# Performance work log

Measured on AMD Instinct MI355X. Metric: run time of the kernel, lower is better.

Reference implementation:

```python
import jax, jax.numpy as jnp
import numpy as np

B, N, D = 4, 8192, 128
H = 4 * D  # exp_factor * features
EPS = 1e-5


def layer_norm(x):
    # fresh nn.LayerNorm each call -> weight=1, bias=0 (no learned affine)
    mu = jnp.mean(x, axis=-1, keepdims=True)
    var = jnp.var(x, axis=-1, keepdims=True)
    return (x - mu) * jax.lax.rsqrt(var + EPS)


def setup_inputs() -> dict:
    key = jax.random.key(0)
    ks = jax.random.split(key, 8)
    x = jax.random.normal(ks[0], (B, N, D), dtype=jnp.float32)
    adj = jax.random.uniform(ks[1], (N, N), dtype=jnp.float32)
    attn_mask = jnp.ones((1,), dtype=jnp.int32)  # unused (torch masked_fill result discarded)
    pad_mask = jnp.ones((1,), dtype=jnp.int32)   # unused
    # FFN params (torch Linear default init scale ~ 1/sqrt(fan_in))
    w1 = jax.random.normal(ks[2], (D, H), dtype=jnp.float32) / np.sqrt(D)
    b1 = jnp.zeros((H,), dtype=jnp.float32)
    w2 = jax.random.normal(ks[3], (H, D), dtype=jnp.float32) / np.sqrt(H)
    b2 = jnp.zeros((D,), dtype=jnp.float32)
    return {"x": x, "adj": adj, "attn_mask": attn_mask, "pad_mask": pad_mask,
            "w1": w1, "b1": b1, "w2": w2, "b2": b2, "dim": 128}


def reference(x, adj, attn_mask, pad_mask, w1, b1, w2, b2, dim):
    # Sublayer 0: x + InrAwaSA(LN(x))
    h = layer_norm(x)                               # [B,N,D]
    # adj is provided -> scores = dense adj, shared across batch.
    # NOTE: masks are no-ops in the source (masked_fill not in-place).
    prob = jax.nn.softmax(adj, axis=-1)             # [N,N]
    attn_out = jnp.einsum('nm,bmd->bnd', prob, h)   # [B,N,D]
    x1 = x + attn_out
    # Sublayer 1: x1 + FFN(LN(x1))
    h1 = layer_norm(x1)
    ffn = jnp.maximum(h1 @ w1 + b1, 0.0) @ w2 + b2
    return x1 + ffn
```

## Files before the change

kernel.cpp:

```cpp
#include <hip/hip_runtime.h>
#include <hip/hip_bf16.h>

typedef __attribute__((ext_vector_type(8))) short bh8;
typedef __attribute__((ext_vector_type(4))) float fx4;
typedef __attribute__((ext_vector_type(8))) int i32x8;
typedef __attribute__((ext_vector_type(4))) int i32x4;

typedef const __attribute__((address_space(1))) unsigned int* gas_p;
typedef __attribute__((address_space(3))) unsigned int* las_p;

#define MFMA(a, b, c) __builtin_amdgcn_mfma_f32_16x16x32_bf16((a), (b), (c), 0, 0, 0)
#define MFMAS(a, b, c) __builtin_amdgcn_mfma_scale_f32_16x16x128_f8f6f4( \
    (a), (b), (c), 0, 0, 0, 0x7f7f7f7f, 0, 0x7f7f7f7f)

__device__ __forceinline__ unsigned short f2bf(float f) {
  unsigned u = __builtin_bit_cast(unsigned, f);
  u += 0x7fff + ((u >> 16) & 1);
  return (unsigned short)(u >> 16);
}

__device__ __forceinline__ float bflo2f(unsigned u) { return __builtin_bit_cast(float, u << 16); }

__device__ __forceinline__ void gld16(const void* g, void* l) {
  __builtin_amdgcn_global_load_lds((gas_p)g, (las_p)l, 16, 0, 0);
}

__global__ __launch_bounds__(256) void transpose_weights(const float* __restrict__ w1,
                                                         const float* __restrict__ w2,
                                                         unsigned short* __restrict__ w1t,
                                                         unsigned short* __restrict__ w2t) {
  const int tgl = blockIdx.x * 256 + threadIdx.x;
  { const int h = tgl >> 7, d = tgl & 127; w1t[tgl] = f2bf(w1[d * 512 + h]); }
  { const int d = tgl >> 9, h = tgl & 511; w2t[tgl] = f2bf(w2[h * 128 + d]); }
}

__global__ __launch_bounds__(256) void ln1_transpose(const float* __restrict__ x,
                                                     unsigned char* __restrict__ htf) {
  const int t = threadIdx.x, lane = t & 63, w = t >> 6;
  const int mt = blockIdx.x, b = blockIdx.y;
  __shared__ unsigned short tile[128 * 64];
  const float* xb = x + ((size_t)b * 8192 + (size_t)mt * 64) * 128;
  for (int it = 0; it < 16; ++it) {
    const int r = w * 16 + it;
    const float2 v = *(const float2*)(xb + r * 128 + lane * 2);
    float s = v.x + v.y, s2 = v.x * v.x + v.y * v.y;
    #pragma unroll
    for (int o = 1; o < 64; o <<= 1) { s += __shfl_xor(s, o); s2 += __shfl_xor(s2, o); }
    const float mean = s * 0.0078125f;
    const float var = s2 * 0.0078125f - mean * mean;
    const float rstd = rsqrtf(var + 1e-5f);
    const int mc = r >> 3, ml = r & 7;
    const int d0 = lane * 2, d1 = d0 + 1;
    tile[d0 * 64 + ((mc ^ (d0 & 7)) << 3) + ml] = f2bf((v.x - mean) * rstd);
    tile[d1 * 64 + ((mc ^ (d1 & 7)) << 3) + ml] = f2bf((v.y - mean) * rstd);
  }
  __syncthreads();
  #pragma unroll
  for (int i = 0; i < 4; ++i) {
    const int idx = i * 256 + t;
    const int d = idx >> 3, mc = idx & 7;
    const bh8 vv = *(const bh8*)(tile + d * 64 + ((mc ^ (d & 7)) << 3));
    int lo = 0, hi = 0;
    lo = __builtin_amdgcn_cvt_pk_fp8_f32(bflo2f((unsigned short)vv[0]),
                                         bflo2f((unsigned short)vv[1]), lo, false);
    lo = __builtin_amdgcn_cvt_pk_fp8_f32(bflo2f((unsigned short)vv[2]),
                                         bflo2f((unsigned short)vv[3]), lo, true);
    hi = __builtin_amdgcn_cvt_pk_fp8_f32(bflo2f((unsigned short)vv[4]),
                                         bflo2f((unsigned short)vv[5]), hi, false);
    hi = __builtin_amdgcn_cvt_pk_fp8_f32(bflo2f((unsigned short)vv[6]),
                                         bflo2f((unsigned short)vv[7]), hi, true);
    const int col = b * 128 + d;
    const int k0 = mt * 64 + mc * 8;
    const int frag = (k0 >> 7) * 32 + (col >> 4);
    const int off = ((col & 15) + 16 * ((k0 >> 5) & 3)) * 32 + (k0 & 31);
    *(uint2*)(htf + (size_t)frag * 2048 + off) = (uint2){(unsigned)lo, (unsigned)hi};
  }
}

__global__ __launch_bounds__(256, 2) void fused_attn(const float* __restrict__ adj,
                                                     const unsigned char* __restrict__ htf,
                                                     unsigned short* __restrict__ pbuf,
                                                     float* __restrict__ sden) {
  const int tid = threadIdx.x, lane = tid & 63, wn = tid >> 6;
  const int mt = blockIdx.x, z = blockIdx.y;
  const int kbase = z * 2048;

  __shared__ unsigned char Al[64 * 128];

  fx4 acc[4][8];
  #pragma unroll
  for (int i = 0; i < 4; ++i)
    #pragma unroll
    for (int j = 0; j < 8; ++j) acc[i][j] = (fx4){0.f, 0.f, 0.f, 0.f};

  i32x8 afr[4];

  const int ar = tid >> 2, aq = tid & 3;
  const float* aroot = adj + (size_t)(mt * 64 + ar) * 8192 + kbase;
  float sacc = 0.f;
  float4 a4[8];
  unsigned pk[8];

  auto issueAdj = [&](int tau) {
    #pragma unroll
    for (int j = 0; j < 8; ++j)
      a4[j] = *(const float4*)(aroot + tau * 128 + aq * 32 + j * 4);
  };
  auto expCvt = [&]() {
    #pragma unroll
    for (int j = 0; j < 8; ++j) {
      const float e0 = __expf(a4[j].x), e1 = __expf(a4[j].y);
      const float e2 = __expf(a4[j].z), e3 = __expf(a4[j].w);
      sacc += (e0 + e1) + (e2 + e3);
      int d = 0;
      d = __builtin_amdgcn_cvt_pk_fp8_f32(e0, e1, d, false);
      d = __builtin_amdgcn_cvt_pk_fp8_f32(e2, e3, d, true);
      pk[j] = (unsigned)d;
    }
  };
  auto writeA = [&]() {
    const i32x4 w0 = (i32x4){(int)pk[0], (int)pk[1], (int)pk[2], (int)pk[3]};
    const i32x4 w1 = (i32x4){(int)pk[4], (int)pk[5], (int)pk[6], (int)pk[7]};
    *(i32x4*)&Al[ar * 128 + (((aq * 2) ^ (ar & 7)) << 4)] = w0;
    *(i32x4*)&Al[ar * 128 + (((aq * 2 + 1) ^ (ar & 7)) << 4)] = w1;
  };
  auto ldAall = [&]() {
    #pragma unroll
    for (int mf = 0; mf < 4; ++mf) {
      const int rr = mf * 16 + (lane & 15);
      const int gb = (lane >> 4) * 2;
      const unsigned char* base = &Al[rr * 128];
      const i32x4 lo = *(const i32x4*)(base + ((gb ^ (rr & 7)) << 4));
      const i32x4 hi = *(const i32x4*)(base + (((gb + 1) ^ (rr & 7)) << 4));
      afr[mf] = (i32x8){lo.x, lo.y, lo.z, lo.w, hi.x, hi.y, hi.z, hi.w};
    }
  };

  issueAdj(0);
  expCvt();
  writeA();
  asm volatile("s_waitcnt lgkmcnt(0)" ::: "memory");
  __builtin_amdgcn_sched_barrier(0);
  __builtin_amdgcn_s_barrier();
  __builtin_amdgcn_sched_barrier(0);

  for (int tt = 0; tt < 16; ++tt) {
    ldAall();
    if (tt < 15) issueAdj(tt + 1);

    const int gkt = z * 16 + tt;
    const unsigned char* fb = htf + ((size_t)gkt * 32 + wn * 8) * 2048 + lane * 32;
    #pragma unroll
    for (int nf = 0; nf < 8; ++nf) {
      const unsigned char* fp = fb + nf * 2048;
      const i32x4 blo = *(const i32x4*)(fp);
      const i32x4 bhi = *(const i32x4*)(fp + 16);
      const i32x8 bfr = (i32x8){blo.x, blo.y, blo.z, blo.w, bhi.x, bhi.y, bhi.z, bhi.w};
      #pragma unroll
      for (int mf = 0; mf < 4; ++mf)
        acc[mf][nf] = MFMAS(afr[mf], bfr, acc[mf][nf]);
    }

    asm volatile("s_waitcnt lgkmcnt(0)" ::: "memory");
    __builtin_amdgcn_sched_barrier(0);
    __builtin_amdgcn_s_barrier();
    __builtin_amdgcn_sched_barrier(0);

    if (tt < 15) {
      expCvt();
      writeA();
      asm volatile("s_waitcnt lgkmcnt(0)" ::: "memory");
      __builtin_amdgcn_sched_barrier(0);
      __builtin_amdgcn_s_barrier();
      __builtin_amdgcn_sched_barrier(0);
    }
  }

  sacc += __shfl_xor(sacc, 1);
  sacc += __shfl_xor(sacc, 2);
  if (aq == 0) sden[(size_t)z * 8192 + mt * 64 + ar] = sacc;

  unsigned short* po = pbuf + (size_t)z * 8192 * 512;
  #pragma unroll
  for (int mf = 0; mf < 4; ++mf)
    #pragma unroll
    for (int nf = 0; nf < 8; ++nf) {
      const int col = wn * 128 + nf * 16 + (lane & 15);
      #pragma unroll
      for (int q = 0; q < 4; ++q) {
        const int row = mt * 64 + mf * 16 + (lane >> 4) * 4 + q;
        po[(size_t)row * 512 + col] = f2bf(acc[mf][nf][q]);
      }
    }
}

#define SWZ16(ks, r) (((((ks) & 7) ^ ((r) & 7)) | ((ks) & 8)))
__global__ __launch_bounds__(512) void ln_ffn_kernel(const float* __restrict__ x,
                                                     const unsigned short* __restrict__ pbuf,
                                                     const float* __restrict__ sden,
                                                     const unsigned short* __restrict__ w1t,
                                                     const unsigned short* __restrict__ w2t,
                                                     const float* __restrict__ b1,
                                                     const float* __restrict__ b2,
                                                     float* __restrict__ out) {
  const int t = threadIdx.x, lane = t & 63, w = t >> 6;
  const int wr = w >> 1, wc = w & 1;
  const int row0 = blockIdx.x * 128;
  __shared__ unsigned short As[128 * 128];
  __shared__ unsigned short W1c[128 * 128];
  __shared__ unsigned short W2c[128 * 128];
  __shared__ unsigned short Ts[128 * 128];

  auto stageW1 = [&](int hc) {
    #pragma unroll
    for (int i = 0; i < 4; ++i) {
      const int idx = i * 512 + t;
      const int row = idx >> 4, kc = idx & 15;
      const int kcs = (kc & 8) | ((kc & 7) ^ (row & 7));
      gld16(w1t + (size_t)(hc * 128 + row) * 128 + kcs * 8, W1c + (idx & ~63) * 8);
    }
  };
  auto stageW2 = [&](int hc) {
    #pragma unroll
    for (int i = 0; i < 4; ++i) {
      const int idx = i * 512 + t;
      const int row = idx >> 4, kc = idx & 15;
      const int kcs = (kc & 8) | ((kc & 7) ^ (row & 7));
      gld16(w2t + (size_t)row * 512 + hc * 128 + kcs * 8, W2c + (idx & ~63) * 8);
    }
  };

  stageW1(0); stageW2(0);

  const int r = t >> 2, q = t & 3, c0 = q * 32;
  const int rowg = row0 + r;
  const int bb = rowg >> 13, nn = rowg & 8191;
  float xv[32];
  {
    const float den = sden[nn] + sden[8192 + nn] + sden[16384 + nn] + sden[24576 + nn];
    const float rinv = 1.f / den;
    const float* xp = x + (size_t)rowg * 128 + c0;
    #pragma unroll
    for (int j = 0; j < 8; ++j) {
      const float4 v4 = *(const float4*)(xp + 4 * j);
      xv[4 * j] = v4.x; xv[4 * j + 1] = v4.y; xv[4 * j + 2] = v4.z; xv[4 * j + 3] = v4.w;
    }
    #pragma unroll
    for (int z = 0; z < 4; ++z) {
      const unsigned short* pp = pbuf + ((size_t)z * 8192 + nn) * 512 + bb * 128 + c0;
      #pragma unroll
      for (int j = 0; j < 4; ++j) {
        const bh8 pv = *(const bh8*)(pp + 8 * j);
        #pragma unroll
        for (int e = 0; e < 8; ++e) xv[8 * j + e] += bflo2f((unsigned short)pv[e]) * rinv;
      }
    }
  }
  float s = 0.f, s2 = 0.f;
  #pragma unroll
  for (int j = 0; j < 32; ++j) { s += xv[j]; s2 += xv[j] * xv[j]; }
  s += __shfl_xor(s, 1); s2 += __shfl_xor(s2, 1);
  s += __shfl_xor(s, 2); s2 += __shfl_xor(s2, 2);
  const float mean = s * 0.0078125f;
  const float var = s2 * 0.0078125f - mean * mean;
  const float rstd = rsqrtf(var + 1e-5f);
  #pragma unroll
  for (int j = 0; j < 4; ++j) {
    const int g = q * 4 + j;
    bh8 pk;
    #pragma unroll
    for (int e = 0; e < 8; ++e) pk[e] = (short)f2bf((xv[8 * j + e] - mean) * rstd);
    *(bh8*)(As + r * 128 + SWZ16(g, r) * 8) = pk;
  }
  __syncthreads();

  fx4 accO[2][4];
  #pragma unroll
  for (int i = 0; i < 2; ++i)
    #pragma unroll
    for (int j = 0; j < 4; ++j) accO[i][j] = (fx4){0.f, 0.f, 0.f, 0.f};

  for (int hc = 0; hc < 4; ++hc) {
    if (hc > 0) stageW2(hc);
    fx4 accT[2][4];
    #pragma unroll
    for (int i = 0; i < 2; ++i)
      #pragma unroll
      for (int j = 0; j < 4; ++j) accT[i][j] = (fx4){0.f, 0.f, 0.f, 0.f};
    #pragma unroll
    for (int kk = 0; kk < 4; ++kk) {
      const int ks = kk * 4 + (lane >> 4);
      bh8 af[2], bfr[4];
      #pragma unroll
      for (int f = 0; f < 2; ++f) {
        const int ra = wr * 32 + f * 16 + (lane & 15);
        af[f] = *(const bh8*)(As + ra * 128 + SWZ16(ks, ra) * 8);
      }
      #pragma unroll
      for (int f = 0; f < 4; ++f) {
        const int rb = wc * 64 + f * 16 + (lane & 15);
        bfr[f] = *(const bh8*)(W1c + rb * 128 + SWZ16(ks, rb) * 8);
      }
      #pragma unroll
      for (int fm = 0; fm < 2; ++fm)
        #pragma unroll
        for (int fn = 0; fn < 4; ++fn) accT[fm][fn] = MFMA(af[fm], bfr[fn], accT[fm][fn]);
    }
    #pragma unroll
    for (int fm = 0; fm < 2; ++fm)
      #pragma unroll
      for (int fn = 0; fn < 4; ++fn) {
        const int col = wc * 64 + fn * 16 + (lane & 15);
        const float bv = b1[hc * 128 + col];
        const int c = col >> 3;
        #pragma unroll
        for (int qq = 0; qq < 4; ++qq) {
          const int row = wr * 32 + fm * 16 + (lane >> 4) * 4 + qq;
          float vv = accT[fm][fn][qq] + bv;
          vv = fmaxf(vv, 0.f);
          Ts[row * 128 + SWZ16(c, row) * 8 + (col & 7)] = f2bf(vv);
        }
      }
    __syncthreads();
    if (hc < 3) {
      stageW1(hc + 1);
    } else {
      float* dst = (r < 64) ? (float*)As + r * 128 + c0 : (float*)W1c + (r - 64) * 128 + c0;
      #pragma unroll
      for (int j = 0; j < 8; ++j)
        *(float4*)(dst + 4 * j) =
            (float4){xv[4 * j], xv[4 * j + 1], xv[4 * j + 2], xv[4 * j + 3]};
    }
    #pragma unroll
    for (int kk = 0; kk < 4; ++kk) {
      const int ks = kk * 4 + (lane >> 4);
      bh8 af[2], bfr[4];
      #pragma unroll
      for (int f = 0; f < 2; ++f) {
        const int ra = wr * 32 + f * 16 + (lane & 15);
        af[f] = *(const bh8*)(Ts + ra * 128 + SWZ16(ks, ra) * 8);
      }
      #pragma unroll
      for (int f = 0; f < 4; ++f) {
        const int rb = wc * 64 + f * 16 + (lane & 15);
        bfr[f] = *(const bh8*)(W2c + rb * 128 + SWZ16(ks, rb) * 8);
      }
      #pragma unroll
      for (int fm = 0; fm < 2; ++fm)
        #pragma unroll
        for (int fn = 0; fn < 4; ++fn) accO[fm][fn] = MFMA(af[fm], bfr[fn], accO[fm][fn]);
    }
    __syncthreads();
  }

  const float* x1a = (const float*)As;
  const float* x1b = (const float*)W1c;
  float* op = out + (size_t)row0 * 128;
  #pragma unroll
  for (int fm = 0; fm < 2; ++fm)
    #pragma unroll
    for (int fn = 0; fn < 4; ++fn) {
      const int col = wc * 64 + fn * 16 + (lane & 15);
      const float bv = b2[col];
      #pragma unroll
      for (int qq = 0; qq < 4; ++qq) {
        const int row = wr * 32 + fm * 16 + (lane >> 4) * 4 + qq;
        const float x1v = (row < 64) ? x1a[row * 128 + col] : x1b[(row - 64) * 128 + col];
        op[row * 128 + col] = x1v + accO[fm][fn][qq] + bv;
      }
    }
}

extern "C" void kernel_launch(void* const* d_in, const int* in_sizes, int n_in,
                              void* d_out, int out_size, void* d_ws, size_t ws_size,
                              hipStream_t stream) {
  const float* x   = (const float*)d_in[0];
  const float* adj = (const float*)d_in[1];
  const float* w1  = (const float*)d_in[4];
  const float* b1  = (const float*)d_in[5];
  const float* w2  = (const float*)d_in[6];
  const float* b2  = (const float*)d_in[7];
  float* out = (float*)d_out;

  char* p = (char*)d_ws;
  unsigned short* w1t  = (unsigned short*)p; p += (size_t)512 * 128 * 2;
  unsigned short* w2t  = (unsigned short*)p; p += (size_t)128 * 512 * 2;
  unsigned char*  htf  = (unsigned char*)p;  p += (size_t)4 * 128 * 8192;
  unsigned short* pbuf = (unsigned short*)p; p += (size_t)4 * 8192 * 512 * 2;
  float*          sden = (float*)p;          p += (size_t)4 * 8192 * 4;

  transpose_weights<<<256, 256, 0, stream>>>(w1, w2, w1t, w2t);
  ln1_transpose<<<dim3(128, 4), 256, 0, stream>>>(x, htf);
  fused_attn<<<dim3(128, 4), 256, 0, stream>>>(adj, htf, pbuf, sden);
  ln_ffn_kernel<<<256, 512, 0, stream>>>(x, pbuf, sden, w1t, w2t, b1, b2, out);
}
```

Measured before the change: 162.9 us.

## Double-buffer adj tile in LDS and prefetch two tiles ahead

Splits the shared A tile into two LDS buffers and keeps two register sets of adj loads, so the next tile's exp/fp8 conversion and LDS write happen during the current tile's MFMA phase. This cuts one barrier per iteration and hides global-load latency by prefetching two k-steps ahead. It also changes the per-thread adj access pattern to interleaved float4 columns, which gives coalesced global reads, and writes LDS as 4-byte stores. The cost is more registers (two float4[8] sets) and twice the LDS, which could hurt occupancy at 2 blocks per CU.

```diff
diff --git a/kernel.cpp b/kernel.cpp
--- a/kernel.cpp
+++ b/kernel.cpp
@@ -85,7 +85,8 @@
   const int mt = blockIdx.x, z = blockIdx.y;
   const int kbase = z * 2048;
 
-  __shared__ unsigned char Al[64 * 128];
+  __shared__ unsigned char Al0[64 * 128];
+  __shared__ unsigned char Al1[64 * 128];
 
   fx4 acc[4][8];
   #pragma unroll
@@ -98,19 +99,19 @@
   const int ar = tid >> 2, aq = tid & 3;
   const float* aroot = adj + (size_t)(mt * 64 + ar) * 8192 + kbase;
   float sacc = 0.f;
-  float4 a4[8];
+  float4 a4a[8], a4b[8];
   unsigned pk[8];
 
-  auto issueAdj = [&](int tau) {
+  auto issueAdj = [&](float4 (&dst)[8], int tau) {
     #pragma unroll
     for (int j = 0; j < 8; ++j)
-      a4[j] = *(const float4*)(aroot + tau * 128 + aq * 32 + j * 4);
-  };
-  auto expCvt = [&]() {
+      dst[j] = *(const float4*)(aroot + tau * 128 + j * 16 + aq * 4);
+  };
+  auto expCvt = [&](const float4 (&src)[8]) {
     #pragma unroll
     for (int j = 0; j < 8; ++j) {
-      const float e0 = __expf(a4[j].x), e1 = __expf(a4[j].y);
-      const float e2 = __expf(a4[j].z), e3 = __expf(a4[j].w);
+      const float e0 = __expf(src[j].x), e1 = __expf(src[j].y);
+      const float e2 = __expf(src[j].z), e3 = __expf(src[j].w);
       sacc += (e0 + e1) + (e2 + e3);
       int d = 0;
       d = __builtin_amdgcn_cvt_pk_fp8_f32(e0, e1, d, false);
@@ -118,36 +119,23 @@
       pk[j] = (unsigned)d;
     }
   };
-  auto writeA = [&]() {
-    const i32x4 w0 = (i32x4){(int)pk[0], (int)pk[1], (int)pk[2], (int)pk[3]};
-    const i32x4 w1 = (i32x4){(int)pk[4], (int)pk[5], (int)pk[6], (int)pk[7]};
-    *(i32x4*)&Al[ar * 128 + (((aq * 2) ^ (ar & 7)) << 4)] = w0;
-    *(i32x4*)&Al[ar * 128 + (((aq * 2 + 1) ^ (ar & 7)) << 4)] = w1;
-  };
-  auto ldAall = [&]() {
+  auto writeA = [&](unsigned char* buf) {
+    #pragma unroll
+    for (int j = 0; j < 8; ++j)
+      *(unsigned*)&buf[ar * 128 + ((j ^ (ar & 7)) << 4) + aq * 4] = pk[j];
+  };
+  auto ldAall = [&](const unsigned char* buf) {
     #pragma unroll
     for (int mf = 0; mf < 4; ++mf) {
       const int rr = mf * 16 + (lane & 15);
       const int gb = (lane >> 4) * 2;
-      const unsigned char* base = &Al[rr * 128];
+      const unsigned char* base = &buf[rr * 128];
       const i32x4 lo = *(const i32x4*)(base + ((gb ^ (rr & 7)) << 4));
       const i32x4 hi = *(const i32x4*)(base + (((gb + 1) ^ (rr & 7)) << 4));
       afr[mf] = (i32x8){lo.x, lo.y, lo.z, lo.w, hi.x, hi.y, hi.z, hi.w};
     }
   };
-
-  issueAdj(0);
-  expCvt();
-  writeA();
-  asm volatile("s_waitcnt lgkmcnt(0)" ::: "memory");
-  __builtin_amdgcn_sched_barrier(0);
-  __builtin_amdgcn_s_barrier();
-  __builtin_amdgcn_sched_barrier(0);
-
-  for (int tt = 0; tt < 16; ++tt) {
-    ldAall();
-    if (tt < 15) issueAdj(tt + 1);
-
+  auto mfmaPhase = [&](int tt) {
     const int gkt = z * 16 + tt;
     const unsigned char* fb = htf + ((size_t)gkt * 32 + wn * 8) * 2048 + lane * 32;
     #pragma unroll
@@ -160,20 +148,35 @@
       for (int mf = 0; mf < 4; ++mf)
         acc[mf][nf] = MFMAS(afr[mf], bfr, acc[mf][nf]);
     }
-
+  };
+  auto body = [&](int tt, unsigned char* bufCur, unsigned char* bufNxt,
+                  float4 (&cur)[8], float4 (&nxt)[8]) {
+    ldAall(bufCur);
+    if (tt + 2 < 16) issueAdj(nxt, tt + 2);
+    if (tt + 1 < 16) {
+      expCvt(cur);
+      writeA(bufNxt);
+    }
+    mfmaPhase(tt);
     asm volatile("s_waitcnt lgkmcnt(0)" ::: "memory");
     __builtin_amdgcn_sched_barrier(0);
     __builtin_amdgcn_s_barrier();
     __builtin_amdgcn_sched_barrier(0);
-
-    if (tt < 15) {
-      expCvt();
-      writeA();
-      asm volatile("s_waitcnt lgkmcnt(0)" ::: "memory");
-      __builtin_amdgcn_sched_barrier(0);
-      __builtin_amdgcn_s_barrier();
-      __builtin_amdgcn_sched_barrier(0);
-    }
+  };
+
+  issueAdj(a4a, 0);
+  expCvt(a4a);
+  writeA(Al0);
+  issueAdj(a4a, 1);
+  asm volatile("s_waitcnt lgkmcnt(0)" ::: "memory");
+  __builtin_amdgcn_sched_barrier(0);
+  __builtin_amdgcn_s_barrier();
+  __builtin_amdgcn_sched_barrier(0);
+
+  for (int i = 0; i < 8; ++i) {
+    const int t0 = 2 * i;
+    body(t0, Al0, Al1, a4a, a4b);
+    body(t0 + 1, Al1, Al0, a4b, a4a);
   }
 
   sacc += __shfl_xor(sacc, 1);
```

Result: slower. 376.8 us (+131.4%).

## Stage adj tiles into double-buffered LDS via async global-to-LDS loads

Applied to the files above, without the earlier changes.

The adj tile loads move from register float4 loads to global_load_lds copies into a double-buffered fp32 LDS staging area with a swizzled layout, prefetched two tiles ahead. The fp8 A-tile buffer is also double-buffered, so the exp/convert step for the next tile runs in the same iteration as the MFMA phase for the current one, leaving one barrier per iteration instead of two. The goal is to hide adj load latency and cut synchronisation. In exchange it uses about 80KB of LDS per block, which could limit occupancy. Each wave only waits on its own vmcnt before reading staging rows that other waves filled, which risks a cross-wave race.

```diff
diff --git a/kernel.cpp b/kernel.cpp
--- a/kernel.cpp
+++ b/kernel.cpp
@@ -85,7 +85,8 @@
   const int mt = blockIdx.x, z = blockIdx.y;
   const int kbase = z * 2048;
 
-  __shared__ unsigned char Al[64 * 128];
+  __shared__ float Ar[2][64 * 128];
+  __shared__ unsigned char Al[2][64 * 128];
 
   fx4 acc[4][8];
   #pragma unroll
@@ -96,21 +97,28 @@
   i32x8 afr[4];
 
   const int ar = tid >> 2, aq = tid & 3;
-  const float* aroot = adj + (size_t)(mt * 64 + ar) * 8192 + kbase;
   float sacc = 0.f;
-  float4 a4[8];
   unsigned pk[8];
 
-  auto issueAdj = [&](int tau) {
-    #pragma unroll
-    for (int j = 0; j < 8; ++j)
-      a4[j] = *(const float4*)(aroot + tau * 128 + aq * 32 + j * 4);
-  };
-  auto expCvt = [&]() {
+  auto issueAr = [&](int buf, int tau) {
+    const int l = tid & 63, wid = tid >> 6;
+    #pragma unroll
+    for (int c = 0; c < 8; ++c) {
+      const int r = c * 8 + wid * 2 + (l >> 5);
+      const int p = l & 31;
+      const float* src = adj + (size_t)(mt * 64 + r) * 8192 + kbase + tau * 128
+                         + ((p ^ (r & 7)) << 2);
+      gld16(src, (char*)&Ar[buf][0] + c * 4096 + wid * 1024);
+    }
+  };
+  auto expCvt = [&](int buf) {
     #pragma unroll
     for (int j = 0; j < 8; ++j) {
-      const float e0 = __expf(a4[j].x), e1 = __expf(a4[j].y);
-      const float e2 = __expf(a4[j].z), e3 = __expf(a4[j].w);
+      const int g = j * 4 + aq;
+      const float4 v = *(const float4*)((const char*)&Ar[buf][0] + ar * 512 +
+                                        ((g ^ (ar & 7)) << 4));
+      const float e0 = __expf(v.x), e1 = __expf(v.y);
+      const float e2 = __expf(v.z), e3 = __expf(v.w);
       sacc += (e0 + e1) + (e2 + e3);
       int d = 0;
       d = __builtin_amdgcn_cvt_pk_fp8_f32(e0, e1, d, false);
@@ -118,36 +126,23 @@
       pk[j] = (unsigned)d;
     }
   };
-  auto writeA = [&]() {
-    const i32x4 w0 = (i32x4){(int)pk[0], (int)pk[1], (int)pk[2], (int)pk[3]};
-    const i32x4 w1 = (i32x4){(int)pk[4], (int)pk[5], (int)pk[6], (int)pk[7]};
-    *(i32x4*)&Al[ar * 128 + (((aq * 2) ^ (ar & 7)) << 4)] = w0;
-    *(i32x4*)&Al[ar * 128 + (((aq * 2 + 1) ^ (ar & 7)) << 4)] = w1;
-  };
-  auto ldAall = [&]() {
+  auto writeA = [&](int buf) {
+    #pragma unroll
+    for (int j = 0; j < 8; ++j)
+      *(unsigned*)&Al[buf][ar * 128 + ((j ^ (ar & 7)) << 4) + aq * 4] = pk[j];
+  };
+  auto ldAall = [&](int buf) {
     #pragma unroll
     for (int mf = 0; mf < 4; ++mf) {
       const int rr = mf * 16 + (lane & 15);
       const int gb = (lane >> 4) * 2;
-      const unsigned char* base = &Al[rr * 128];
+      const unsigned char* base = &Al[buf][rr * 128];
       const i32x4 lo = *(const i32x4*)(base + ((gb ^ (rr & 7)) << 4));
       const i32x4 hi = *(const i32x4*)(base + (((gb + 1) ^ (rr & 7)) << 4));
       afr[mf] = (i32x8){lo.x, lo.y, lo.z, lo.w, hi.x, hi.y, hi.z, hi.w};
     }
   };
-
-  issueAdj(0);
-  expCvt();
-  writeA();
-  asm volatile("s_waitcnt lgkmcnt(0)" ::: "memory");
-  __builtin_amdgcn_sched_barrier(0);
-  __builtin_amdgcn_s_barrier();
-  __builtin_amdgcn_sched_barrier(0);
-
-  for (int tt = 0; tt < 16; ++tt) {
-    ldAall();
-    if (tt < 15) issueAdj(tt + 1);
-
+  auto mfmaPhase = [&](int tt) {
     const int gkt = z * 16 + tt;
     const unsigned char* fb = htf + ((size_t)gkt * 32 + wn * 8) * 2048 + lane * 32;
     #pragma unroll
@@ -160,21 +155,44 @@
       for (int mf = 0; mf < 4; ++mf)
         acc[mf][nf] = MFMAS(afr[mf], bfr, acc[mf][nf]);
     }
-
+  };
+  auto body = [&](int tt, bool doIssue, bool doConv) {
+    const int cur = tt & 1;
+    if (doIssue) issueAr(cur, tt + 2);
+    ldAall(cur);
+    mfmaPhase(tt);
+    if (doConv) {
+      if (doIssue) { asm volatile("s_waitcnt vmcnt(8)" ::: "memory"); }
+      else         { asm volatile("s_waitcnt vmcnt(0)" ::: "memory"); }
+      __builtin_amdgcn_sched_barrier(0);
+      expCvt(cur ^ 1);
+      writeA(cur ^ 1);
+    }
     asm volatile("s_waitcnt lgkmcnt(0)" ::: "memory");
     __builtin_amdgcn_sched_barrier(0);
     __builtin_amdgcn_s_barrier();
     __builtin_amdgcn_sched_barrier(0);
-
-    if (tt < 15) {
-      expCvt();
-      writeA();
-      asm volatile("s_waitcnt lgkmcnt(0)" ::: "memory");
-      __builtin_amdgcn_sched_barrier(0);
-      __builtin_amdgcn_s_barrier();
-      __builtin_amdgcn_sched_barrier(0);
-    }
-  }
+  };
+
+  issueAr(0, 0);
+  issueAr(1, 1);
+  asm volatile("s_waitcnt vmcnt(8)" ::: "memory");
+  __builtin_amdgcn_sched_barrier(0);
+  __builtin_amdgcn_s_barrier();
+  __builtin_amdgcn_sched_barrier(0);
+  expCvt(0);
+  writeA(0);
+  asm volatile("s_waitcnt lgkmcnt(0)" ::: "memory");
+  __builtin_amdgcn_sched_barrier(0);
+  __builtin_amdgcn_s_barrier();
+  __builtin_amdgcn_sched_barrier(0);
+
+  for (int i = 0; i < 7; ++i) {
+    body(2 * i, true, true);
+    body(2 * i + 1, true, true);
+  }
+  body(14, false, true);
+  body(15, false, false);
 
   sacc += __shfl_xor(sacc, 1);
   sacc += __shfl_xor(sacc, 2);
```

Result: faster. 150.3 us (median of 2 runs) (-7.7%).

## Split softmax into separate fp8 fragment kernel and barrier-free attention GEMM

Applied to the files above, without the earlier changes.

Moves the exp/normalise/fp8-pack of the adjacency matrix into a standalone row-softmax kernel that writes probabilities pre-scaled by 4096 in MFMA fragment layout. The attention GEMM then loads A fragments straight from global memory with no LDS staging or barriers, and rescales on output. The per-row denominator buffer and its use in the FFN kernel are removed. This adds a 64 MB intermediate write and read plus an extra launch, in exchange for decoupling the exp work from the MFMA loop.

```diff
diff --git a/kernel.cpp b/kernel.cpp
--- a/kernel.cpp
+++ b/kernel.cpp
@@ -77,15 +77,52 @@
   }
 }
 
-__global__ __launch_bounds__(256, 2) void fused_attn(const float* __restrict__ adj,
-                                                     const unsigned char* __restrict__ htf,
-                                                     unsigned short* __restrict__ pbuf,
-                                                     float* __restrict__ sden) {
+__global__ __launch_bounds__(256) void softmax_frag(const float* __restrict__ adj,
+                                                    unsigned char* __restrict__ probf) {
+  const int t = threadIdx.x, lane = t & 63, w = t >> 6;
+  const size_t n = blockIdx.x;
+  __shared__ float red[4];
+  __shared__ unsigned char sp[8192];
+  const fx4* row = (const fx4*)(adj + n * 8192);
+  fx4 v[8];
+  float lsum = 0.f;
+  #pragma unroll
+  for (int i = 0; i < 8; ++i) {
+    const fx4 a = row[i * 256 + t];
+    fx4 e;
+    e.x = __expf(a.x); e.y = __expf(a.y); e.z = __expf(a.z); e.w = __expf(a.w);
+    v[i] = e;
+    lsum += e.x + e.y + e.z + e.w;
+  }
+  #pragma unroll
+  for (int o = 1; o < 64; o <<= 1) lsum += __shfl_xor(lsum, o);
+  if (lane == 0) red[w] = lsum;
+  __syncthreads();
+  const float rinv = 4096.f / (red[0] + red[1] + red[2] + red[3]);
+  #pragma unroll
+  for (int i = 0; i < 8; ++i) {
+    int pk = 0;
+    pk = __builtin_amdgcn_cvt_pk_fp8_f32(v[i].x * rinv, v[i].y * rinv, pk, false);
+    pk = __builtin_amdgcn_cvt_pk_fp8_f32(v[i].z * rinv, v[i].w * rinv, pk, true);
+    const int g = 64 * i + (t >> 2);
+    const int pg = g ^ ((g >> 4) & 7);
+    *(unsigned*)&sp[pg * 16 + (t & 3) * 4] = (unsigned)pk;
+  }
+  __syncthreads();
+  const int g0 = 2 * t, g1 = 2 * t + 1;
+  const i32x4 q0 = *(const i32x4*)&sp[(g0 ^ ((g0 >> 4) & 7)) * 16];
+  const i32x4 q1 = *(const i32x4*)&sp[(g1 ^ ((g1 >> 4) & 7)) * 16];
+  unsigned char* dst = probf + (((n >> 4) * 64 + (t >> 2)) * 2048)
+                     + (((int)(n & 15) + 16 * (t & 3)) * 32);
+  *(i32x4*)dst = q0;
+  *(i32x4*)(dst + 16) = q1;
+}
+
+__global__ __launch_bounds__(256, 2) void attn_gemm(const unsigned char* __restrict__ probf,
+                                                    const unsigned char* __restrict__ htf,
+                                                    unsigned short* __restrict__ pbuf) {
   const int tid = threadIdx.x, lane = tid & 63, wn = tid >> 6;
   const int mt = blockIdx.x, z = blockIdx.y;
-  const int kbase = z * 2048;
-
-  __shared__ unsigned char Al[64 * 128];
 
   fx4 acc[4][8];
   #pragma unroll
@@ -93,93 +130,30 @@
     #pragma unroll
     for (int j = 0; j < 8; ++j) acc[i][j] = (fx4){0.f, 0.f, 0.f, 0.f};
 
-  i32x8 afr[4];
-
-  const int ar = tid >> 2, aq = tid & 3;
-  const float* aroot = adj + (size_t)(mt * 64 + ar) * 8192 + kbase;
-  float sacc = 0.f;
-  float4 a4[8];
-  unsigned pk[8];
-
-  auto issueAdj = [&](int tau) {
-    #pragma unroll
-    for (int j = 0; j < 8; ++j)
-      a4[j] = *(const float4*)(aroot + tau * 128 + aq * 32 + j * 4);
-  };
-  auto expCvt = [&]() {
-    #pragma unroll
-    for (int j = 0; j < 8; ++j) {
-      const float e0 = __expf(a4[j].x), e1 = __expf(a4[j].y);
-      const float e2 = __expf(a4[j].z), e3 = __expf(a4[j].w);
-      sacc += (e0 + e1) + (e2 + e3);
-      int d = 0;
-      d = __builtin_amdgcn_cvt_pk_fp8_f32(e0, e1, d, false);
-      d = __builtin_amdgcn_cvt_pk_fp8_f32(e2, e3, d, true);
-      pk[j] = (unsigned)d;
-    }
-  };
-  auto writeA = [&]() {
-    const i32x4 w0 = (i32x4){(int)pk[0], (int)pk[1], (int)pk[2], (int)pk[3]};
-    const i32x4 w1 = (i32x4){(int)pk[4], (int)pk[5], (int)pk[6], (int)pk[7]};
-    *(i32x4*)&Al[ar * 128 + (((aq * 2) ^ (ar & 7)) << 4)] = w0;
-    *(i32x4*)&Al[ar * 128 + (((aq * 2 + 1) ^ (ar & 7)) << 4)] = w1;
-  };
-  auto ldAall = [&]() {
+  for (int tt = 0; tt < 16; ++tt) {
+    const int gkt = z * 16 + tt;
+    i32x8 afr[4];
     #pragma unroll
     for (int mf = 0; mf < 4; ++mf) {
-      const int rr = mf * 16 + (lane & 15);
-      const int gb = (lane >> 4) * 2;
-      const unsigned char* base = &Al[rr * 128];
-      const i32x4 lo = *(const i32x4*)(base + ((gb ^ (rr & 7)) << 4));
-      const i32x4 hi = *(const i32x4*)(base + (((gb + 1) ^ (rr & 7)) << 4));
+      const unsigned char* ap =
+          probf + ((size_t)((mt * 4 + mf) * 64 + gkt)) * 2048 + lane * 32;
+      const i32x4 lo = *(const i32x4*)ap;
+      const i32x4 hi = *(const i32x4*)(ap + 16);
       afr[mf] = (i32x8){lo.x, lo.y, lo.z, lo.w, hi.x, hi.y, hi.z, hi.w};
     }
-  };
-
-  issueAdj(0);
-  expCvt();
-  writeA();
-  asm volatile("s_waitcnt lgkmcnt(0)" ::: "memory");
-  __builtin_amdgcn_sched_barrier(0);
-  __builtin_amdgcn_s_barrier();
-  __builtin_amdgcn_sched_barrier(0);
-
-  for (int tt = 0; tt < 16; ++tt) {
-    ldAall();
-    if (tt < 15) issueAdj(tt + 1);
-
-    const int gkt = z * 16 + tt;
     const unsigned char* fb = htf + ((size_t)gkt * 32 + wn * 8) * 2048 + lane * 32;
     #pragma unroll
     for (int nf = 0; nf < 8; ++nf) {
-      const unsigned char* fp = fb + nf * 2048;
-      const i32x4 blo = *(const i32x4*)(fp);
-      const i32x4 bhi = *(const i32x4*)(fp + 16);
+      const i32x4 blo = *(const i32x4*)(fb + nf * 2048);
+      const i32x4 bhi = *(const i32x4*)(fb + nf * 2048 + 16);
       const i32x8 bfr = (i32x8){blo.x, blo.y, blo.z, blo.w, bhi.x, bhi.y, bhi.z, bhi.w};
       #pragma unroll
       for (int mf = 0; mf < 4; ++mf)
         acc[mf][nf] = MFMAS(afr[mf], bfr, acc[mf][nf]);
     }
-
-    asm volatile("s_waitcnt lgkmcnt(0)" ::: "memory");
-    __builtin_amdgcn_sched_barrier(0);
-    __builtin_amdgcn_s_barrier();
-    __builtin_amdgcn_sched_barrier(0);
-
-    if (tt < 15) {
-      expCvt();
-      writeA();
-      asm volatile("s_waitcnt lgkmcnt(0)" ::: "memory");
-      __builtin_amdgcn_sched_barrier(0);
-      __builtin_amdgcn_s_barrier();
-      __builtin_amdgcn_sched_barrier(0);
-    }
-  }
-
-  sacc += __shfl_xor(sacc, 1);
-  sacc += __shfl_xor(sacc, 2);
-  if (aq == 0) sden[(size_t)z * 8192 + mt * 64 + ar] = sacc;
-
+  }
+
+  const float ds = 0.000244140625f;
   unsigned short* po = pbuf + (size_t)z * 8192 * 512;
   #pragma unroll
   for (int mf = 0; mf < 4; ++mf)
@@ -189,7 +163,7 @@
       #pragma unroll
       for (int q = 0; q < 4; ++q) {
         const int row = mt * 64 + mf * 16 + (lane >> 4) * 4 + q;
-        po[(size_t)row * 512 + col] = f2bf(acc[mf][nf][q]);
+        po[(size_t)row * 512 + col] = f2bf(acc[mf][nf][q] * ds);
       }
     }
 }
@@ -197,7 +171,6 @@
 #define SWZ16(ks, r) (((((ks) & 7) ^ ((r) & 7)) | ((ks) & 8)))
 __global__ __launch_bounds__(512) void ln_ffn_kernel(const float* __restrict__ x,
                                                      const unsigned short* __restrict__ pbuf,
-                                                     const float* __restrict__ sden,
                                                      const unsigned short* __restrict__ w1t,
                                                      const unsigned short* __restrict__ w2t,
                                                      const float* __restrict__ b1,
@@ -237,8 +210,6 @@
   const int bb = rowg >> 13, nn = rowg & 8191;
   float xv[32];
   {
-    const float den = sden[nn] + sden[8192 + nn] + sden[16384 + nn] + sden[24576 + nn];
-    const float rinv = 1.f / den;
     const float* xp = x + (size_t)rowg * 128 + c0;
     #pragma unroll
     for (int j = 0; j < 8; ++j) {
@@ -252,7 +223,7 @@
       for (int j = 0; j < 4; ++j) {
         const bh8 pv = *(const bh8*)(pp + 8 * j);
         #pragma unroll
-        for (int e = 0; e < 8; ++e) xv[8 * j + e] += bflo2f((unsigned short)pv[e]) * rinv;
+        for (int e = 0; e < 8; ++e) xv[8 * j + e] += bflo2f((unsigned short)pv[e]);
       }
     }
   }
@@ -387,10 +358,11 @@
   unsigned short* w2t  = (unsigned short*)p; p += (size_t)128 * 512 * 2;
   unsigned char*  htf  = (unsigned char*)p;  p += (size_t)4 * 128 * 8192;
   unsigned short* pbuf = (unsigned short*)p; p += (size_t)4 * 8192 * 512 * 2;
-  float*          sden = (float*)p;          p += (size_t)4 * 8192 * 4;
+  unsigned char*  probf = (unsigned char*)p; p += (size_t)8192 * 8192;
 
   transpose_weights<<<256, 256, 0, stream>>>(w1, w2, w1t, w2t);
   ln1_transpose<<<dim3(128, 4), 256, 0, stream>>>(x, htf);
-  fused_attn<<<dim3(128, 4), 256, 0, stream>>>(adj, htf, pbuf, sden);
-  ln_ffn_kernel<<<256, 512, 0, stream>>>(x, pbuf, sden, w1t, w2t, b1, b2, out);
-}
+  softmax_frag<<<8192, 256, 0, stream>>>(adj, probf);
+  attn_gemm<<<dim3(128, 4), 256, 0, stream>>>(probf, htf, pbuf);
+  ln_ffn_kernel<<<256, 512, 0, stream>>>(x, pbuf, w1t, w2t, b1, b2, out);
+}
```

After: 186.0 us. 14.2% more time.
